# Kernel tuning notes

Measured on AMD Instinct MI355X. Metric: run time of the kernel, lower is better.

The kernel has to match this reference:

```python
import jax, jax.numpy as jnp
import numpy as np

N = 50000      # num nodes
E = 800000     # num edges (before self-loops)
IN = 256       # in_channels
HID = 64       # hidden_channels
H = 4          # heads
D = HID * H    # concatenated hidden dim
NEG = 0.2      # LeakyReLU negative slope (PyG GATConv default)
OUT_EDGE = 3


def setup_inputs() -> dict:
    key = jax.random.key(0)
    ks = jax.random.split(key, 16)
    def glorot(k, shape, fan):
        return (jax.random.normal(k, shape, jnp.float32) / np.float32(np.sqrt(fan)))
    x = jax.random.normal(ks[0], (N, IN), jnp.float32)
    edge_index = jax.random.randint(ks[1], (2, E), 0, N, dtype=jnp.int64)
    # GAT layer 1
    W1 = glorot(ks[2], (IN, H * HID), IN)
    a1_src = glorot(ks[3], (H, HID), HID)
    a1_dst = glorot(ks[4], (H, HID), HID)
    b1 = jnp.zeros((H * HID,), jnp.float32)
    # GAT layer 2
    W2 = glorot(ks[5], (D, H * HID), D)
    a2_src = glorot(ks[6], (H, HID), HID)
    a2_dst = glorot(ks[7], (H, HID), HID)
    b2 = jnp.zeros((H * HID,), jnp.float32)
    # node predictor (Linear D -> 1)
    Wn = glorot(ks[8], (D, 1), D)
    bn = jnp.zeros((1,), jnp.float32)
    # edge predictor (Bilinear D x D -> 3)
    Wb = glorot(ks[9], (OUT_EDGE, D, D), D)
    bb = jnp.zeros((OUT_EDGE,), jnp.float32)
    return dict(x=x, edge_index=edge_index, W1=W1, a1_src=a1_src, a1_dst=a1_dst, b1=b1,
                W2=W2, a2_src=a2_src, a2_dst=a2_dst, b2=b2, Wn=Wn, bn=bn, Wb=Wb, bb=bb)


def _gat_layer(x, row, col, W, a_src, a_dst, b):
    """PyG-style GATConv (concat=True, eval mode). row=source, col=target."""
    heads, C = a_src.shape
    xw = (x @ W).reshape(-1, heads, C)                       # [N, H, C]
    s_src = jnp.einsum('nhc,hc->nh', xw, a_src)              # [N, H]
    s_dst = jnp.einsum('nhc,hc->nh', xw, a_dst)              # [N, H]
    logits = jax.nn.leaky_relu(s_src[row] + s_dst[col], NEG)  # [Etot, H]
    # segment-softmax over incoming edges of each target node
    m = jax.ops.segment_max(logits, col, num_segments=N)     # [N, H]
    m = jnp.where(jnp.isfinite(m), m, 0.0)
    ex = jnp.exp(logits - m[col])                            # [Etot, H]
    den = jax.ops.segment_sum(ex, col, num_segments=N)       # [N, H] (>0: self-loops)
    alpha = ex / den[col]                                    # [Etot, H]
    out = jax.ops.segment_sum(alpha[:, :, None] * xw[row], col, num_segments=N)  # [N,H,C]
    return out.reshape(-1, heads * C) + b, alpha


def reference(x, edge_index, W1, a1_src, a1_dst, b1, W2, a2_src, a2_dst, b2, Wn, bn, Wb, bb):
    row0, col0 = edge_index[0], edge_index[1]
    loops = jnp.arange(N, dtype=edge_index.dtype)            # add_self_loops=True (PyG default)
    row = jnp.concatenate([row0, loops])
    col = jnp.concatenate([col0, loops])
    h, alpha1 = _gat_layer(x, row, col, W1, a1_src, a1_dst, b1)
    h = jax.nn.elu(h)
    h, alpha2 = _gat_layer(h, row, col, W2, a2_src, a2_dst, b2)
    h = jax.nn.elu(h)                                        # [N, D] final embeddings
    node_preds = (h @ Wn + bn).squeeze(-1)                   # [N]
    edge_preds = jnp.einsum('ed,odf,ef->eo', h[row0], Wb, h[col0]) + bb  # [E, 3]
    attn_weights = (alpha1.mean(axis=1) + alpha2.mean(axis=1)) / 2.0     # [E+N]
    return node_preds, edge_preds, h, attn_weights
```

## Files before the change

kernel.cpp:

```cpp
#include <hip/hip_runtime.h>
#include <hip/hip_bf16.h>

#define N_NODES 50000
#define N_EDGES 800000
#define ETOT    (N_EDGES + N_NODES)
#define NALL    (ETOT + N_EDGES)
#define DIM     256
#define NEG_SLOPE 0.2f
#define NBLK2   ((2 * N_NODES + 255) / 256)

#define AS1 __attribute__((address_space(1)))
#define AS3 __attribute__((address_space(3)))

typedef __attribute__((ext_vector_type(4))) float  floatx4;
typedef __attribute__((ext_vector_type(8))) short  shortx8;
typedef __attribute__((ext_vector_type(4))) short  shortx4;

__device__ inline float bf2f(unsigned short u) {
    union { unsigned int i; float f; } c; c.i = ((unsigned int)u) << 16; return c.f;
}
__device__ inline unsigned short f2bf(float x) {
    union { float f; unsigned int i; } c; c.f = x;
    unsigned int r = c.i + 0x7FFF + ((c.i >> 16) & 1);
    return (unsigned short)(r >> 16);
}

__global__ void detect_params(const unsigned short* __restrict__ xs,
                              const int* __restrict__ ei, int* __restrict__ flags,
                              const void* s0, const void* s1, const void* s2,
                              const void* s3, const void* s4, const void* s5,
                              const void* s6, const void* s7, const void* s8,
                              unsigned short* __restrict__ dst) {
    int tid = threadIdx.x;
    unsigned short s = xs[2 * tid];
    float av = fabsf(bf2f(s));
    int hit = (av > 0.001f && av < 100.0f) ? 1 : 0;
    int odd = ei[2 * tid + 1];
    __shared__ int sh_hit[256], sh_nz[256];
    __shared__ int sh_f0;
    sh_hit[tid] = hit; sh_nz[tid] = (odd != 0) ? 1 : 0;
    __syncthreads();
    for (int st = 128; st > 0; st >>= 1) {
        if (tid < st) { sh_hit[tid] += sh_hit[tid + st]; sh_nz[tid] += sh_nz[tid + st]; }
        __syncthreads();
    }
    if (tid == 0) {
        int f0 = (sh_hit[0] < 128) ? 1 : 0;
        flags[0] = f0;
        flags[1] = (sh_nz[0] == 0) ? 1 : 0;
        sh_f0 = f0;
    }
    __syncthreads();
    int fp32 = sh_f0;
    const void* srcs[9] = { s0, s1, s2, s3, s4, s5, s6, s7, s8 };
    const int   offs[9] = { 0, 256, 512, 768, 1024, 1280, 1536, 1792, 1793 };
    const int   cnts[9] = { 256, 256, 256, 256, 256, 256, 256, 1, 3 };
#pragma unroll
    for (int sg = 0; sg < 9; sg++) {
        if (tid < cnts[sg]) {
            dst[offs[sg] + tid] = fp32 ? f2bf(((const float*)srcs[sg])[tid])
                                       : ((const unsigned short*)srcs[sg])[tid];
        }
    }
}

__global__ void norm_x(const void* __restrict__ src, unsigned short* __restrict__ dst,
                       const int* __restrict__ flags) {
    int i = (blockIdx.x * 256 + threadIdx.x) * 4;
    if (flags[0]) {
        const float* s = (const float*)src;
        dst[i + 0] = f2bf(s[i + 0]); dst[i + 1] = f2bf(s[i + 1]);
        dst[i + 2] = f2bf(s[i + 2]); dst[i + 3] = f2bf(s[i + 3]);
    } else {
        *(shortx4*)(dst + i) = *(const shortx4*)((const unsigned short*)src + i);
    }
}

__global__ void norm_edges(const int* __restrict__ ei, int* __restrict__ rown,
                           int* __restrict__ coln, const int* __restrict__ flags,
                           int* __restrict__ cnt2,
                           int* __restrict__ rankd, int* __restrict__ ranks) {
    int e = blockIdx.x * 256 + threadIdx.x;
    if (e >= N_EDGES) return;
    int r, c;
    if (flags[1]) { r = ei[2 * e]; c = ei[2 * (N_EDGES + e)]; }
    else          { r = ei[e];     c = ei[N_EDGES + e]; }
    rown[e] = r; coln[e] = c;
    rankd[e] = atomicAdd(&cnt2[c], 1);
    ranks[e] = atomicAdd(&cnt2[N_NODES + r], 1);
}

__global__ void transpose_kernel(const void* __restrict__ W1, const void* __restrict__ W2,
                                 const void* __restrict__ Wb, unsigned short* __restrict__ BT,
                                 const int* __restrict__ flags) {
    int idx = blockIdx.x * 256 + threadIdx.x;
    int m = idx >> 16, rem = idx & 65535;
    int k = rem >> 8, nn = rem & 255;
    const void* src = (m == 0) ? W1 : ((m == 1) ? W2 : Wb);
    size_t el = (m >= 2) ? ((size_t)(m - 2) * 65536 + rem) : (size_t)rem;
    unsigned short val = flags[0] ? f2bf(((const float*)src)[el])
                                  : ((const unsigned short*)src)[el];
    BT[(size_t)m * 65536 + nn * 256 + k] = val;
}

__global__ void init_cnt(int* __restrict__ p) {
    int i = blockIdx.x * 256 + threadIdx.x;
    if (i < 2 * N_NODES) p[i] = (i < N_NODES) ? 1 : 0;
}

__global__ void scan_part(const int* __restrict__ cnt, int* __restrict__ part, int n) {
    __shared__ int sh[256];
    int t = threadIdx.x;
    int i = blockIdx.x * 256 + t;
    sh[t] = (i < n) ? cnt[i] : 0;
    __syncthreads();
    for (int s = 128; s > 0; s >>= 1) {
        if (t < s) sh[t] += sh[t + s];
        __syncthreads();
    }
    if (t == 0) part[blockIdx.x] = sh[0];
}

__global__ void scan_small512(int* __restrict__ part, int n) {
    __shared__ int sh[512];
    int t = threadIdx.x;
    int v = (t < n) ? part[t] : 0;
    sh[t] = v;
    __syncthreads();
    for (int s = 1; s < 512; s <<= 1) {
        int u = (t >= s) ? sh[t - s] : 0;
        __syncthreads();
        sh[t] += u;
        __syncthreads();
    }
    if (t < n) part[t] = sh[t] - v;
}

__global__ void scan_final(const int* __restrict__ cnt, const int* __restrict__ part,
                           int* __restrict__ off, int n, int total,
                           int2* __restrict__ slot) {
    __shared__ int sh[256];
    int t = threadIdx.x;
    int i = blockIdx.x * 256 + t;
    int v = (i < n) ? cnt[i] : 0;
    sh[t] = v;
    __syncthreads();
    for (int s = 1; s < 256; s <<= 1) {
        int u = (t >= s) ? sh[t - s] : 0;
        __syncthreads();
        sh[t] += u;
        __syncthreads();
    }
    if (i < n) {
        int o = part[blockIdx.x] + sh[t] - v;
        off[i] = o;
        if (i < N_NODES) slot[o] = make_int2(N_EDGES + i, i);
    }
    if (i == 0) off[n] = total;
}

__global__ void fill_edges(const int* __restrict__ coln, const int* __restrict__ rown,
                           const int* __restrict__ off2,
                           const int* __restrict__ rankd, const int* __restrict__ ranks,
                           int2* __restrict__ slot) {
    int e = blockIdx.x * 256 + threadIdx.x;
    if (e >= N_EDGES) return;
    int c = coln[e], r = rown[e];
    int od = off2[c];
    int os = off2[N_NODES + r];
    slot[od + rankd[e]] = make_int2(e, r);
    slot[os + ranks[e]] = make_int2(e, c);
}

__global__ __launch_bounds__(256) void gemm256(
    const unsigned short* __restrict__ A,
    const unsigned short* __restrict__ BT,
    unsigned short* __restrict__ Cb, int M, int Nc)
{
    __shared__ short As[128 * 32];
    __shared__ short Bs[128 * 32];
    int ncol = Nc >> 7;
    int lin = blockIdx.x;
    int xcd = lin & 7, sl = lin >> 3;
    int rowq = sl / ncol;
    int row = xcd + 8 * rowq;
    int col = sl - rowq * ncol;
    if (row * 128 >= M) return;
    int m0 = row * 128, n0 = col * 128;
    int tid = threadIdx.x, lane = tid & 63, wave = tid >> 6;
    int wm = wave & 1, wn = wave >> 1;
    floatx4 acc[4][4] = {};
    for (int k0 = 0; k0 < 256; k0 += 32) {
        __syncthreads();
#pragma unroll
        for (int i = 0; i < 2; i++) {
            int c = i * 256 + tid;
            int rowl = c >> 2, koff = (c & 3) * 8;
            int gr = m0 + rowl; if (gr > M - 1) gr = M - 1;
            __builtin_amdgcn_global_load_lds(
                (const AS1 unsigned int*)(A + (size_t)gr * 256 + k0 + koff),
                (AS3 unsigned int*)(As + c * 8), 16, 0, 0);
            int gn = n0 + rowl;
            __builtin_amdgcn_global_load_lds(
                (const AS1 unsigned int*)(BT + (size_t)gn * 256 + k0 + koff),
                (AS3 unsigned int*)(Bs + c * 8), 16, 0, 0);
        }
        __syncthreads();
        shortx8 af[4], bfr[4];
#pragma unroll
        for (int mt = 0; mt < 4; mt++)
            af[mt] = *(const shortx8*)(As + (wm * 64 + mt * 16 + (lane & 15)) * 32 + (lane >> 4) * 8);
#pragma unroll
        for (int nt = 0; nt < 4; nt++)
            bfr[nt] = *(const shortx8*)(Bs + (wn * 64 + nt * 16 + (lane & 15)) * 32 + (lane >> 4) * 8);
#pragma unroll
        for (int mt = 0; mt < 4; mt++)
#pragma unroll
            for (int nt = 0; nt < 4; nt++)
                acc[mt][nt] = __builtin_amdgcn_mfma_f32_16x16x32_bf16(af[mt], bfr[nt], acc[mt][nt], 0, 0, 0);
    }
#pragma unroll
    for (int mt = 0; mt < 4; mt++) {
#pragma unroll
        for (int r = 0; r < 4; r++) {
            int grow = m0 + wm * 64 + mt * 16 + (lane >> 4) * 4 + r;
            if (grow >= M) continue;
#pragma unroll
            for (int nt = 0; nt < 4; nt++) {
                int gcol = n0 + wn * 64 + nt * 16 + (lane & 15);
                Cb[(size_t)grow * Nc + gcol] = f2bf(acc[mt][nt][r]);
            }
        }
    }
}

__global__ __launch_bounds__(256) void s_kernel(
    const unsigned short* __restrict__ xw,
    const unsigned short* __restrict__ a_src,
    const unsigned short* __restrict__ a_dst,
    float* __restrict__ s_src, float* __restrict__ s_dst)
{
    int wid = (blockIdx.x * 256 + threadIdx.x) >> 6;
    int lane = threadIdx.x & 63;
    if (wid >= N_NODES) return;
    int f = lane * 4;
    shortx4 xv = *(const shortx4*)(xw + (size_t)wid * DIM + f);
    shortx4 asv = *(const shortx4*)(a_src + f);
    shortx4 adv = *(const shortx4*)(a_dst + f);
    float x0 = bf2f((unsigned short)xv.x), x1 = bf2f((unsigned short)xv.y);
    float x2 = bf2f((unsigned short)xv.z), x3 = bf2f((unsigned short)xv.w);
    float ps = x0 * bf2f((unsigned short)asv.x) + x1 * bf2f((unsigned short)asv.y)
             + x2 * bf2f((unsigned short)asv.z) + x3 * bf2f((unsigned short)asv.w);
    float pd = x0 * bf2f((unsigned short)adv.x) + x1 * bf2f((unsigned short)adv.y)
             + x2 * bf2f((unsigned short)adv.z) + x3 * bf2f((unsigned short)adv.w);
    for (int s = 1; s < 16; s <<= 1) { ps += __shfl_xor(ps, s); pd += __shfl_xor(pd, s); }
    if ((lane & 15) == 0) {
        int h = lane >> 4;
        s_src[(size_t)wid * 4 + h] = ps;
        s_dst[(size_t)wid * 4 + h] = pd;
    }
}

__global__ __launch_bounds__(256) void attn_agg(
    const unsigned short* __restrict__ xw,
    const float* __restrict__ s_src, const float* __restrict__ s_dst,
    const int* __restrict__ off, const int2* __restrict__ slot,
    const unsigned short* __restrict__ bias,
    unsigned short* __restrict__ h_bf, float* __restrict__ h_f32,
    float* __restrict__ attn_acc, float* __restrict__ attn_out,
    const unsigned short* __restrict__ wn, const unsigned short* __restrict__ bn,
    float* __restrict__ node_out, int layer)
{
    int wid = (blockIdx.x * 256 + threadIdx.x) >> 6;
    int lane = threadIdx.x & 63;
    if (wid >= N_NODES) return;
    int n = wid;
    int g = lane >> 4, gl = lane & 15;
    float sd = s_dst[(size_t)n * 4 + g];
    int base = off[n];
    int deg = off[n + 1] - base;

    float t0c = -1e30f, t1c = -1e30f;
    int r0c, r1c;
    {
        int i0 = gl < deg ? gl : deg - 1;
        int i1 = (16 + gl) < deg ? (16 + gl) : deg - 1;
        r0c = slot[base + i0].y;
        r1c = slot[base + i1].y;
        float s0 = s_src[(size_t)r0c * 4 + g];
        float s1 = s_src[(size_t)r1c * 4 + g];
        float u0 = s0 + sd; u0 = u0 > 0.f ? u0 : NEG_SLOPE * u0;
        float u1 = s1 + sd; u1 = u1 > 0.f ? u1 : NEG_SLOPE * u1;
        if (gl < deg)        t0c = u0;
        if ((16 + gl) < deg) t1c = u1;
    }
    float m = fmaxf(t0c, t1c);
    float d = 0.f;
    if (gl < deg)        d += __expf(t0c - m);
    if ((16 + gl) < deg) d += __expf(t1c - m);
    for (int i2 = 32 + gl; i2 < deg; i2 += 16) {
        int r = slot[base + i2].y;
        float s = s_src[(size_t)r * 4 + g];
        float t = s + sd; t = t > 0.f ? t : NEG_SLOPE * t;
        float nm = fmaxf(m, t);
        d = d * __expf(m - nm) + __expf(t - nm);
        m = nm;
    }
#pragma unroll
    for (int s = 1; s < 16; s <<= 1) {
        float om = __shfl_xor(m, s), od = __shfl_xor(d, s);
        float nm = fmaxf(m, om);
        d = d * __expf(m - nm) + od * __expf(om - nm);
        m = nm;
    }
    float inv_d = 1.f / d;

    int f4 = gl * 4;
    floatx4 acc0 = {}, acc1 = {}, acc2 = {}, acc3 = {};
    for (int c0 = 0; c0 < deg; c0 += 16) {
        float a; int r;
        if (c0 == 0)       { r = r0c; a = __expf(t0c - m) * inv_d; }
        else if (c0 == 16) { r = r1c; a = __expf(t1c - m) * inv_d; }
        else {
            int i = c0 + gl;
            int ii = i < deg ? i : deg - 1;
            r = slot[base + ii].y;
            float s = s_src[(size_t)r * 4 + g];
            float t = s + sd; t = t > 0.f ? t : NEG_SLOPE * t;
            a = (i < deg) ? __expf(t - m) * inv_d : 0.f;
        }
        int i = c0 + gl;
        float asum = a + __shfl_xor(a, 16);
        asum += __shfl_xor(asum, 32);
        if (g == 0 && i < deg) {
            float suma = 0.125f * asum;
            if (layer == 0) attn_acc[base + i] = suma;
            else            attn_out[slot[base + i].x] = attn_acc[base + i] + suma;
        }
        int cnt = deg - c0; if (cnt > 16) cnt = 16;
        for (int k4 = 0; k4 < cnt; k4 += 4) {
            int j = k4 + g;
            int jj = j < cnt ? j : cnt - 1;
            int rj  = __shfl(r, jj);
            float a0 = __shfl(a, jj);
            float a1 = __shfl(a, 16 | jj);
            float a2 = __shfl(a, 32 | jj);
            float a3 = __shfl(a, 48 | jj);
            if (j >= cnt) { a0 = 0.f; a1 = 0.f; a2 = 0.f; a3 = 0.f; }
            const unsigned short* rp = xw + (size_t)rj * DIM + f4;
            shortx4 x0 = *(const shortx4*)(rp + 0);
            shortx4 x1 = *(const shortx4*)(rp + 64);
            shortx4 x2 = *(const shortx4*)(rp + 128);
            shortx4 x3 = *(const shortx4*)(rp + 192);
            acc0.x += a0 * bf2f((unsigned short)x0.x);
            acc0.y += a0 * bf2f((unsigned short)x0.y);
            acc0.z += a0 * bf2f((unsigned short)x0.z);
            acc0.w += a0 * bf2f((unsigned short)x0.w);
            acc1.x += a1 * bf2f((unsigned short)x1.x);
            acc1.y += a1 * bf2f((unsigned short)x1.y);
            acc1.z += a1 * bf2f((unsigned short)x1.z);
            acc1.w += a1 * bf2f((unsigned short)x1.w);
            acc2.x += a2 * bf2f((unsigned short)x2.x);
            acc2.y += a2 * bf2f((unsigned short)x2.y);
            acc2.z += a2 * bf2f((unsigned short)x2.z);
            acc2.w += a2 * bf2f((unsigned short)x2.w);
            acc3.x += a3 * bf2f((unsigned short)x3.x);
            acc3.y += a3 * bf2f((unsigned short)x3.y);
            acc3.z += a3 * bf2f((unsigned short)x3.z);
            acc3.w += a3 * bf2f((unsigned short)x3.w);
        }
    }
    int h1 = lane & 32;
    floatx4 sendA = h1 ? acc0 : acc2;
    floatx4 sendB = h1 ? acc1 : acc3;
    floatx4 keepA = h1 ? acc2 : acc0;
    floatx4 keepB = h1 ? acc3 : acc1;
    keepA.x += __shfl_xor(sendA.x, 32); keepA.y += __shfl_xor(sendA.y, 32);
    keepA.z += __shfl_xor(sendA.z, 32); keepA.w += __shfl_xor(sendA.w, 32);
    keepB.x += __shfl_xor(sendB.x, 32); keepB.y += __shfl_xor(sendB.y, 32);
    keepB.z += __shfl_xor(sendB.z, 32); keepB.w += __shfl_xor(sendB.w, 32);
    int p = lane & 16;
    floatx4 send2 = p ? keepA : keepB;
    floatx4 accw  = p ? keepB : keepA;
    accw.x += __shfl_xor(send2.x, 16); accw.y += __shfl_xor(send2.y, 16);
    accw.z += __shfl_xor(send2.z, 16); accw.w += __shfl_xor(send2.w, 16);

    int f = lane * 4;
    shortx4 bv = *(const shortx4*)(bias + f);
    float o0 = accw.x + bf2f((unsigned short)bv.x);
    float o1 = accw.y + bf2f((unsigned short)bv.y);
    float o2 = accw.z + bf2f((unsigned short)bv.z);
    float o3 = accw.w + bf2f((unsigned short)bv.w);
    o0 = o0 > 0.f ? o0 : (__expf(o0) - 1.f);
    o1 = o1 > 0.f ? o1 : (__expf(o1) - 1.f);
    o2 = o2 > 0.f ? o2 : (__expf(o2) - 1.f);
    o3 = o3 > 0.f ? o3 : (__expf(o3) - 1.f);
    if (h_bf) {
        shortx4 pk;
        pk.x = (short)f2bf(o0); pk.y = (short)f2bf(o1);
        pk.z = (short)f2bf(o2); pk.w = (short)f2bf(o3);
        *(shortx4*)(h_bf + (size_t)n * DIM + f) = pk;
    }
    if (h_f32) {
        floatx4 pv; pv.x = o0; pv.y = o1; pv.z = o2; pv.w = o3;
        *(floatx4*)(h_f32 + (size_t)n * DIM + f) = pv;
    }
    if (wn) {
        shortx4 wv = *(const shortx4*)(wn + f);
        float p2 = o0 * bf2f((unsigned short)wv.x) + o1 * bf2f((unsigned short)wv.y)
                 + o2 * bf2f((unsigned short)wv.z) + o3 * bf2f((unsigned short)wv.w);
        for (int s = 1; s < 64; s <<= 1) p2 += __shfl_xor(p2, s);
        if (lane == 0) node_out[n] = p2 + bf2f(bn[0]);
    }
}

__global__ __launch_bounds__(256) void edge_pred_mfma(
    const unsigned short* __restrict__ h,
    const unsigned short* __restrict__ V,
    const int* __restrict__ soff, const int2* __restrict__ slot,
    const unsigned short* __restrict__ bb, float* __restrict__ outp)
{
    int wid = (blockIdx.x * 256 + threadIdx.x) >> 6;
    int lane = threadIdx.x & 63;
    if (wid >= N_NODES) return;
    int s = wid;
    int base = soff[s];
    int deg = soff[s + 1] - base;
    if (deg == 0) return;

    int c  = lane & 15;
    int kg = lane >> 4;
    int cc = c < 3 ? c : 2;

    const unsigned short* vb = V + (size_t)s * 768 + cc * 256 + kg * 8;
    shortx8 bfrag[8];
#pragma unroll
    for (int kk = 0; kk < 8; kk++)
        bfrag[kk] = *(const shortx8*)(vb + kk * 32);
    float bias_c = bf2f(bb[cc]);

    for (int ch = 0; ch < deg; ch += 16) {
        int i = ch + c;
        int ii = i < deg ? i : deg - 1;
        int t = slot[base + ii].y;
        const unsigned short* ha = h + (size_t)t * DIM + kg * 8;
        shortx8 afr[8];
#pragma unroll
        for (int kk = 0; kk < 8; kk++)
            afr[kk] = *(const shortx8*)(ha + kk * 32);
        floatx4 acc;
        acc.x = bias_c; acc.y = bias_c; acc.z = bias_c; acc.w = bias_c;
#pragma unroll
        for (int kk = 0; kk < 8; kk++)
            acc = __builtin_amdgcn_mfma_f32_16x16x32_bf16(afr[kk], bfrag[kk], acc, 0, 0, 0);
        if (c < 3) {
#pragma unroll
            for (int r = 0; r < 4; r++) {
                int iw = ch + kg * 4 + r;
                if (iw < deg) {
                    int e = slot[base + iw].x;
                    outp[(size_t)e * 3 + c] = acc[r];
                }
            }
        }
    }
}

extern "C" void kernel_launch(void* const* d_in, const int* in_sizes, int n_in,
                              void* d_out, int out_size, void* d_ws, size_t ws_size,
                              hipStream_t stream) {
    const void* x_raw  = d_in[0];
    const int*  ei_raw = (const int*)d_in[1];
    float* out = (float*)d_out;

    char* w = (char*)d_ws;
    size_t off_b = 0;
    auto alloc = [&](size_t bytes) -> char* {
        char* p = w + off_b; off_b = (off_b + bytes + 255) & ~(size_t)255; return p;
    };
    int*            flags  = (int*)alloc(256);
    unsigned short* buf0   = (unsigned short*)alloc((size_t)N_NODES * DIM * 2);
    unsigned short* R      = (unsigned short*)alloc((size_t)N_NODES * 768 * 2);
    unsigned short* buf1   = R;
    unsigned short* buf2   = R + (size_t)N_NODES * DIM;
    unsigned short* V      = R;
    float*          ssrc   = (float*)alloc((size_t)N_NODES * 4 * 4);
    float*          sdst   = (float*)alloc((size_t)N_NODES * 4 * 4);
    float*          attn   = (float*)alloc((size_t)ETOT * 4);
    int*            cnt2   = (int*)alloc((size_t)2 * N_NODES * 4);
    int*            off2   = (int*)alloc((size_t)(2 * N_NODES + 1) * 4);
    int*            part   = (int*)alloc(512 * 4);
    int2*           slot   = (int2*)alloc((size_t)NALL * 8);
    int*            rankd  = (int*)alloc((size_t)N_EDGES * 4);
    int*            ranks  = (int*)alloc((size_t)N_EDGES * 4);
    int*            rown   = (int*)alloc((size_t)N_EDGES * 4);
    int*            coln   = (int*)alloc((size_t)N_EDGES * 4);
    unsigned short* BT     = (unsigned short*)alloc((size_t)5 * 65536 * 2);
    unsigned short* small  = (unsigned short*)alloc(2048 * 2);

    float* out_node = out;
    float* out_edge = out + 50000;
    float* out_h    = out + 2450000;
    float* out_attn = out + 15250000;

    int e0b = (N_EDGES + 255) / 256;
    int node_wave_blocks = (N_NODES * 64) / 256;
    int nrow = (N_NODES + 127) / 128;
    int slots_per_xcd = (nrow + 7) / 8;
    int gg = slots_per_xcd * 8 * 2;
    int gv = slots_per_xcd * 8 * 6;

    detect_params<<<1, 256, 0, stream>>>((const unsigned short*)x_raw, ei_raw, flags,
                                         d_in[3], d_in[4], d_in[5], d_in[7], d_in[8],
                                         d_in[9], d_in[10], d_in[11], d_in[13], small);
    norm_x<<<12500, 256, 0, stream>>>(x_raw, buf0, flags);
    init_cnt<<<(2 * N_NODES + 255) / 256, 256, 0, stream>>>(cnt2);
    norm_edges<<<e0b, 256, 0, stream>>>(ei_raw, rown, coln, flags, cnt2, rankd, ranks);
    transpose_kernel<<<1280, 256, 0, stream>>>(d_in[2], d_in[6], d_in[12], BT, flags);

    scan_part<<<NBLK2, 256, 0, stream>>>(cnt2, part, 2 * N_NODES);
    scan_small512<<<1, 512, 0, stream>>>(part, NBLK2);
    scan_final<<<NBLK2, 256, 0, stream>>>(cnt2, part, off2, 2 * N_NODES, NALL, slot);
    fill_edges<<<e0b, 256, 0, stream>>>(coln, rown, off2, rankd, ranks, slot);

    gemm256<<<gg, 256, 0, stream>>>(buf0, BT, buf1, N_NODES, 256);
    s_kernel<<<node_wave_blocks, 256, 0, stream>>>(buf1, small + 0, small + 256, ssrc, sdst);
    attn_agg<<<node_wave_blocks, 256, 0, stream>>>(buf1, ssrc, sdst, off2, slot,
                                                   small + 512, buf2, nullptr, attn, nullptr,
                                                   nullptr, nullptr, nullptr, 0);

    gemm256<<<gg, 256, 0, stream>>>(buf2, BT + 65536, buf1, N_NODES, 256);
    s_kernel<<<node_wave_blocks, 256, 0, stream>>>(buf1, small + 768, small + 1024, ssrc, sdst);
    attn_agg<<<node_wave_blocks, 256, 0, stream>>>(buf1, ssrc, sdst, off2, slot,
                                                   small + 1280, buf0, out_h, attn, out_attn,
                                                   small + 1536, small + 1792, out_node, 1);

    gemm256<<<gv, 256, 0, stream>>>(buf0, BT + 2 * 65536, V, N_NODES, 768);
    edge_pred_mfma<<<node_wave_blocks, 256, 0, stream>>>(buf0, V, off2 + N_NODES,
                                                         slot, small + 1793, out_edge);
}
```

Measured before the change: 564.6 us.

## Fuse attention score computation into GEMM epilogue and drop softmax max pass

Removes the separate s_kernel by computing the per-head source and destination attention scores directly from the GEMM accumulators in the epilogue, using shuffles across the 16-column lane groups. Separately, attn_agg no longer tracks a running max for the segment softmax and exponentiates the raw logits. This saves a kernel launch, a re-read of xw, and the online-softmax rescaling work. Unshifted exp can overflow or lose precision for large logits, and the scores now come from fp32 accumulators rather than bf16-rounded xw, so results differ slightly.

```diff
diff --git a/kernel.cpp b/kernel.cpp
--- a/kernel.cpp
+++ b/kernel.cpp
@@ -175,7 +175,9 @@
 __global__ __launch_bounds__(256) void gemm256(
     const unsigned short* __restrict__ A,
     const unsigned short* __restrict__ BT,
-    unsigned short* __restrict__ Cb, int M, int Nc)
+    unsigned short* __restrict__ Cb, int M, int Nc,
+    float* __restrict__ ssrc, float* __restrict__ sdst,
+    const unsigned short* __restrict__ asrc, const unsigned short* __restrict__ adst)
 {
     __shared__ short As[128 * 32];
     __shared__ short Bs[128 * 32];
@@ -232,32 +234,35 @@
             }
         }
     }
-}
-
-__global__ __launch_bounds__(256) void s_kernel(
-    const unsigned short* __restrict__ xw,
-    const unsigned short* __restrict__ a_src,
-    const unsigned short* __restrict__ a_dst,
-    float* __restrict__ s_src, float* __restrict__ s_dst)
-{
-    int wid = (blockIdx.x * 256 + threadIdx.x) >> 6;
-    int lane = threadIdx.x & 63;
-    if (wid >= N_NODES) return;
-    int f = lane * 4;
-    shortx4 xv = *(const shortx4*)(xw + (size_t)wid * DIM + f);
-    shortx4 asv = *(const shortx4*)(a_src + f);
-    shortx4 adv = *(const shortx4*)(a_dst + f);
-    float x0 = bf2f((unsigned short)xv.x), x1 = bf2f((unsigned short)xv.y);
-    float x2 = bf2f((unsigned short)xv.z), x3 = bf2f((unsigned short)xv.w);
-    float ps = x0 * bf2f((unsigned short)asv.x) + x1 * bf2f((unsigned short)asv.y)
-             + x2 * bf2f((unsigned short)asv.z) + x3 * bf2f((unsigned short)asv.w);
-    float pd = x0 * bf2f((unsigned short)adv.x) + x1 * bf2f((unsigned short)adv.y)
-             + x2 * bf2f((unsigned short)adv.z) + x3 * bf2f((unsigned short)adv.w);
-    for (int s = 1; s < 16; s <<= 1) { ps += __shfl_xor(ps, s); pd += __shfl_xor(pd, s); }
-    if ((lane & 15) == 0) {
-        int h = lane >> 4;
-        s_src[(size_t)wid * 4 + h] = ps;
-        s_dst[(size_t)wid * 4 + h] = pd;
+    if (asrc) {
+        int h = (n0 >> 6) + wn;
+        float as_v[4], ad_v[4];
+#pragma unroll
+        for (int nt = 0; nt < 4; nt++) {
+            int gcol = n0 + wn * 64 + nt * 16 + (lane & 15);
+            as_v[nt] = bf2f(asrc[gcol]);
+            ad_v[nt] = bf2f(adst[gcol]);
+        }
+#pragma unroll
+        for (int mt = 0; mt < 4; mt++) {
+#pragma unroll
+            for (int r = 0; r < 4; r++) {
+                int grow = m0 + wm * 64 + mt * 16 + (lane >> 4) * 4 + r;
+                float ps = acc[mt][0][r] * as_v[0] + acc[mt][1][r] * as_v[1]
+                         + acc[mt][2][r] * as_v[2] + acc[mt][3][r] * as_v[3];
+                float pd = acc[mt][0][r] * ad_v[0] + acc[mt][1][r] * ad_v[1]
+                         + acc[mt][2][r] * ad_v[2] + acc[mt][3][r] * ad_v[3];
+#pragma unroll
+                for (int sft = 1; sft < 16; sft <<= 1) {
+                    ps += __shfl_xor(ps, sft);
+                    pd += __shfl_xor(pd, sft);
+                }
+                if ((lane & 15) == 0 && grow < M) {
+                    ssrc[(size_t)grow * 4 + h] = ps;
+                    sdst[(size_t)grow * 4 + h] = pd;
+                }
+            }
+        }
     }
 }
 
@@ -280,7 +285,7 @@
     int base = off[n];
     int deg = off[n + 1] - base;
 
-    float t0c = -1e30f, t1c = -1e30f;
+    float e0c = 0.f, e1c = 0.f;
     int r0c, r1c;
     {
         int i0 = gl < deg ? gl : deg - 1;
@@ -291,43 +296,33 @@
         float s1 = s_src[(size_t)r1c * 4 + g];
         float u0 = s0 + sd; u0 = u0 > 0.f ? u0 : NEG_SLOPE * u0;
         float u1 = s1 + sd; u1 = u1 > 0.f ? u1 : NEG_SLOPE * u1;
-        if (gl < deg)        t0c = u0;
-        if ((16 + gl) < deg) t1c = u1;
-    }
-    float m = fmaxf(t0c, t1c);
-    float d = 0.f;
-    if (gl < deg)        d += __expf(t0c - m);
-    if ((16 + gl) < deg) d += __expf(t1c - m);
+        if (gl < deg)        e0c = __expf(u0);
+        if ((16 + gl) < deg) e1c = __expf(u1);
+    }
+    float d = e0c + e1c;
     for (int i2 = 32 + gl; i2 < deg; i2 += 16) {
         int r = slot[base + i2].y;
         float s = s_src[(size_t)r * 4 + g];
         float t = s + sd; t = t > 0.f ? t : NEG_SLOPE * t;
-        float nm = fmaxf(m, t);
-        d = d * __expf(m - nm) + __expf(t - nm);
-        m = nm;
-    }
-#pragma unroll
-    for (int s = 1; s < 16; s <<= 1) {
-        float om = __shfl_xor(m, s), od = __shfl_xor(d, s);
-        float nm = fmaxf(m, om);
-        d = d * __expf(m - nm) + od * __expf(om - nm);
-        m = nm;
-    }
+        d += __expf(t);
+    }
+#pragma unroll
+    for (int s = 1; s < 16; s <<= 1) d += __shfl_xor(d, s);
     float inv_d = 1.f / d;
 
     int f4 = gl * 4;
     floatx4 acc0 = {}, acc1 = {}, acc2 = {}, acc3 = {};
     for (int c0 = 0; c0 < deg; c0 += 16) {
         float a; int r;
-        if (c0 == 0)       { r = r0c; a = __expf(t0c - m) * inv_d; }
-        else if (c0 == 16) { r = r1c; a = __expf(t1c - m) * inv_d; }
+        if (c0 == 0)       { r = r0c; a = e0c * inv_d; }
+        else if (c0 == 16) { r = r1c; a = e1c * inv_d; }
         else {
             int i = c0 + gl;
             int ii = i < deg ? i : deg - 1;
             r = slot[base + ii].y;
             float s = s_src[(size_t)r * 4 + g];
             float t = s + sd; t = t > 0.f ? t : NEG_SLOPE * t;
-            a = (i < deg) ? __expf(t - m) * inv_d : 0.f;
+            a = (i < deg) ? __expf(t) * inv_d : 0.f;
         }
         int i = c0 + gl;
         float asum = a + __shfl_xor(a, 16);
@@ -523,19 +518,20 @@
     scan_final<<<NBLK2, 256, 0, stream>>>(cnt2, part, off2, 2 * N_NODES, NALL, slot);
     fill_edges<<<e0b, 256, 0, stream>>>(coln, rown, off2, rankd, ranks, slot);
 
-    gemm256<<<gg, 256, 0, stream>>>(buf0, BT, buf1, N_NODES, 256);
-    s_kernel<<<node_wave_blocks, 256, 0, stream>>>(buf1, small + 0, small + 256, ssrc, sdst);
+    gemm256<<<gg, 256, 0, stream>>>(buf0, BT, buf1, N_NODES, 256,
+                                    ssrc, sdst, small + 0, small + 256);
     attn_agg<<<node_wave_blocks, 256, 0, stream>>>(buf1, ssrc, sdst, off2, slot,
                                                    small + 512, buf2, nullptr, attn, nullptr,
                                                    nullptr, nullptr, nullptr, 0);
 
-    gemm256<<<gg, 256, 0, stream>>>(buf2, BT + 65536, buf1, N_NODES, 256);
-    s_kernel<<<node_wave_blocks, 256, 0, stream>>>(buf1, small + 768, small + 1024, ssrc, sdst);
+    gemm256<<<gg, 256, 0, stream>>>(buf2, BT + 65536, buf1, N_NODES, 256,
+                                    ssrc, sdst, small + 768, small + 1024);
     attn_agg<<<node_wave_blocks, 256, 0, stream>>>(buf1, ssrc, sdst, off2, slot,
                                                    small + 1280, buf0, out_h, attn, out_attn,
                                                    small + 1536, small + 1792, out_node, 1);
 
-    gemm256<<<gv, 256, 0, stream>>>(buf0, BT + 2 * 65536, V, N_NODES, 768);
+    gemm256<<<gv, 256, 0, stream>>>(buf0, BT + 2 * 65536, V, N_NODES, 768,
+                                    nullptr, nullptr, nullptr, nullptr);
     edge_pred_mfma<<<node_wave_blocks, 256, 0, stream>>>(buf0, V, off2 + N_NODES,
                                                          slot, small + 1793, out_edge);
 }
```

Result: no change. 561.1 us (-0.6%).
